# Kernel tuning notes

Measured on AMD Instinct MI355X. Metric: run time of the kernel, lower is better.

Reference implementation:

```python
import jax, jax.numpy as jnp
import numpy as np

B, N, C, K = 8, 18432, 1024, 1024  # scenes, points(=V*576 tokens), feat dim, num_sample_tokens
VOXEL_SIZE = 0.2


def setup_inputs() -> dict:
    rng = np.random.default_rng(0)
    # room-scale point cloud, ~0.2m voxels -> substantial pooling
    xyz = rng.uniform(-3.0, 3.0, size=(B, N, 3)).astype(np.float32)
    vox = np.floor(xyz / VOXEL_SIZE).astype(np.int64)
    p2v = np.zeros((B, N), dtype=np.int32)
    counts = []
    for b in range(B):  # host-side preprocessing (mirrors torch voxelize hash+unique)
        h = vox[b, :, 0] * 1_000_000 + vox[b, :, 1] * 1_000 + vox[b, :, 2]
        _, inv = np.unique(h, return_inverse=True)
        p2v[b] = inv.astype(np.int32)
        counts.append(int(inv.max()) + 1)
    S = max(counts)  # static segment count (>= per-batch voxel counts)
    # per-batch random resample over that batch's occupied voxels (np.random.choice in source)
    resample = np.stack([
        rng.choice(counts[b], size=K, replace=counts[b] < K) for b in range(B)
    ]).astype(np.int32)
    feats = jax.random.normal(jax.random.key(0), (B, N, C), dtype=jnp.float32)
    return {
        "video_features": feats,
        "p2v": jnp.asarray(p2v),
        "resample_idx": jnp.asarray(resample),
        "num_segments": S,
    }


def reference(video_features, p2v, resample_idx, num_segments):
    # scatter_mean per batch: sum features per voxel / point count per voxel
    def pool_one(f, seg):  # f: [N, C], seg: [N]
        sums = jax.ops.segment_sum(f, seg, num_segments=num_segments)          # [S, C]
        cnt = jax.ops.segment_sum(jnp.ones((f.shape[0],), f.dtype), seg,
                                  num_segments=num_segments)                    # [S]
        return sums / jnp.maximum(cnt, 1.0)[:, None]

    means = jax.vmap(pool_one)(video_features, p2v)                             # [B, S, C]
    # fixed-size resample gather -> [B, K, C]
    out = jnp.take_along_axis(means, resample_idx[..., None].astype(jnp.int32), axis=1)
    return out
```

## Files before the change

### kernel.cpp

```cpp
#include <hip/hip_runtime.h>

#define BATCH 8
#define NPTS  18432
#define CH    1024
#define KOUT  1024
#define MAXS  18432
#define CAP   64

__global__ void scatter_map_kernel(const int* __restrict__ resample,
                                   int* __restrict__ map) {
    int i = blockIdx.x * blockDim.x + threadIdx.x;
    if (i >= BATCH * KOUT) return;
    int b = i / KOUT;
    int vox = resample[i];
    map[b * MAXS + vox] = i - b * KOUT;
}

__global__ void build_lists_kernel(const int* __restrict__ p2v,
                                   const int* __restrict__ map,
                                   int* __restrict__ counts,
                                   int* __restrict__ lists) {
    int i = blockIdx.x * blockDim.x + threadIdx.x;
    if (i >= BATCH * NPTS) return;
    int b = i / NPTS;
    int vox = p2v[i];
    int slot = map[b * MAXS + vox];
    if (slot < 0) return;
    int row = b * KOUT + slot;
    int pos = atomicAdd(&counts[row], 1);
    if (pos < CAP) lists[row * CAP + pos] = i;
}

__global__ void gather_mean_kernel(const float* __restrict__ feats,
                                   const int* __restrict__ counts,
                                   const int* __restrict__ lists,
                                   float* __restrict__ out) {
    int row = blockIdx.x;
    int cnt = counts[row];
    int n = cnt < CAP ? cnt : CAP;
    float4 acc = make_float4(0.f, 0.f, 0.f, 0.f);
    for (int j = 0; j < n; ++j) {
        int pt = lists[row * CAP + j];
        float4 v = ((const float4*)(feats + (size_t)pt * CH))[threadIdx.x];
        acc.x += v.x; acc.y += v.y; acc.z += v.z; acc.w += v.w;
    }
    float inv = 1.0f / (float)(cnt > 0 ? cnt : 1);
    acc.x *= inv; acc.y *= inv; acc.z *= inv; acc.w *= inv;
    ((float4*)(out + (size_t)row * CH))[threadIdx.x] = acc;
}

extern "C" void kernel_launch(void* const* d_in, const int* in_sizes, int n_in,
                              void* d_out, int out_size, void* d_ws, size_t ws_size,
                              hipStream_t stream) {
    const float* feats    = (const float*)d_in[0];
    const int*   p2v      = (const int*)  d_in[1];
    const int*   resample = (const int*)  d_in[2];
    float* out = (float*)d_out;

    int* map    = (int*)d_ws;
    int* counts = map + BATCH * MAXS;
    int* lists  = counts + BATCH * KOUT;

    hipMemsetAsync(map,    0xFF, (size_t)BATCH * MAXS * sizeof(int), stream);
    hipMemsetAsync(counts, 0,    (size_t)BATCH * KOUT * sizeof(int), stream);

    scatter_map_kernel<<<(BATCH * KOUT + 255) / 256, 256, 0, stream>>>(resample, map);

    build_lists_kernel<<<(BATCH * NPTS + 255) / 256, 256, 0, stream>>>(
        p2v, map, counts, lists);

    gather_mean_kernel<<<BATCH * KOUT, 256, 0, stream>>>(feats, counts, lists, out);
}
```

Before: 669.3 us.

## Fuse map, list build and gather into one cooperative persistent kernel

Replaces two memsets and three kernel launches with a single cooperative kernel. It initializes the workspace, builds the voxel map, builds the point lists and performs the gather-mean, separated by grid-wide syncs. The gather now assigns one wave per output row with four float4 accumulators per lane. This removes launch and memset overheads and raises memory-level parallelism, at the cost of grid-sync latency and a fixed persistent grid size.

Result: slower. 929.1 us (+38.8%).

```diff
diff --git a/kernel.cpp b/kernel.cpp
--- a/kernel.cpp
+++ b/kernel.cpp
@@ -1,4 +1,7 @@
 #include <hip/hip_runtime.h>
+#include <hip/hip_cooperative_groups.h>
+
+namespace cg = cooperative_groups;
 
 #define BATCH 8
 #define NPTS  18432
@@ -7,46 +10,75 @@
 #define MAXS  18432
 #define CAP   64
 
-__global__ void scatter_map_kernel(const int* __restrict__ resample,
-                                   int* __restrict__ map) {
-    int i = blockIdx.x * blockDim.x + threadIdx.x;
-    if (i >= BATCH * KOUT) return;
-    int b = i / KOUT;
-    int vox = resample[i];
-    map[b * MAXS + vox] = i - b * KOUT;
-}
+#define GRID_BLOCKS   1024
+#define BLOCK_THREADS 256
 
-__global__ void build_lists_kernel(const int* __restrict__ p2v,
-                                   const int* __restrict__ map,
-                                   int* __restrict__ counts,
-                                   int* __restrict__ lists) {
-    int i = blockIdx.x * blockDim.x + threadIdx.x;
-    if (i >= BATCH * NPTS) return;
-    int b = i / NPTS;
-    int vox = p2v[i];
-    int slot = map[b * MAXS + vox];
-    if (slot < 0) return;
-    int row = b * KOUT + slot;
-    int pos = atomicAdd(&counts[row], 1);
-    if (pos < CAP) lists[row * CAP + pos] = i;
-}
+__global__ __launch_bounds__(BLOCK_THREADS, 4)
+void fused_pool_kernel(const float* __restrict__ feats,
+                       const int*   __restrict__ p2v,
+                       const int*   __restrict__ resample,
+                       int*         __restrict__ map,
+                       int*         __restrict__ counts,
+                       int*         __restrict__ lists,
+                       float*       __restrict__ out) {
+    cg::grid_group grid = cg::this_grid();
+    const int tid      = blockIdx.x * BLOCK_THREADS + threadIdx.x;
+    const int nthreads = GRID_BLOCKS * BLOCK_THREADS;
 
-__global__ void gather_mean_kernel(const float* __restrict__ feats,
-                                   const int* __restrict__ counts,
-                                   const int* __restrict__ lists,
-                                   float* __restrict__ out) {
-    int row = blockIdx.x;
-    int cnt = counts[row];
-    int n = cnt < CAP ? cnt : CAP;
-    float4 acc = make_float4(0.f, 0.f, 0.f, 0.f);
-    for (int j = 0; j < n; ++j) {
-        int pt = lists[row * CAP + j];
-        float4 v = ((const float4*)(feats + (size_t)pt * CH))[threadIdx.x];
-        acc.x += v.x; acc.y += v.y; acc.z += v.z; acc.w += v.w;
+    for (int i = tid; i < BATCH * MAXS; i += nthreads) map[i] = -1;
+    for (int i = tid; i < BATCH * KOUT; i += nthreads) counts[i] = 0;
+    grid.sync();
+
+    for (int i = tid; i < BATCH * KOUT; i += nthreads) {
+        int b = i >> 10;
+        map[b * MAXS + resample[i]] = i & (KOUT - 1);
     }
-    float inv = 1.0f / (float)(cnt > 0 ? cnt : 1);
-    acc.x *= inv; acc.y *= inv; acc.z *= inv; acc.w *= inv;
-    ((float4*)(out + (size_t)row * CH))[threadIdx.x] = acc;
+    grid.sync();
+
+    for (int i = tid; i < BATCH * NPTS; i += nthreads) {
+        int b    = i / NPTS;
+        int slot = map[b * MAXS + p2v[i]];
+        if (slot >= 0) {
+            int row = (b << 10) + slot;
+            int pos = atomicAdd(&counts[row], 1);
+            if (pos < CAP) lists[row * CAP + pos] = i;
+        }
+    }
+    grid.sync();
+
+    const int wid    = tid >> 6;
+    const int lane   = tid & 63;
+    const int nwaves = nthreads >> 6;
+    for (int row = wid; row < BATCH * KOUT; row += nwaves) {
+        int cnt = counts[row];
+        int n   = cnt < CAP ? cnt : CAP;
+        float4 a0 = make_float4(0.f, 0.f, 0.f, 0.f);
+        float4 a1 = make_float4(0.f, 0.f, 0.f, 0.f);
+        float4 a2 = make_float4(0.f, 0.f, 0.f, 0.f);
+        float4 a3 = make_float4(0.f, 0.f, 0.f, 0.f);
+        for (int j = 0; j < n; ++j) {
+            int pt = lists[row * CAP + j];
+            const float4* src = (const float4*)(feats + (size_t)pt * CH);
+            float4 v0 = src[lane];
+            float4 v1 = src[lane + 64];
+            float4 v2 = src[lane + 128];
+            float4 v3 = src[lane + 192];
+            a0.x += v0.x; a0.y += v0.y; a0.z += v0.z; a0.w += v0.w;
+            a1.x += v1.x; a1.y += v1.y; a1.z += v1.z; a1.w += v1.w;
+            a2.x += v2.x; a2.y += v2.y; a2.z += v2.z; a2.w += v2.w;
+            a3.x += v3.x; a3.y += v3.y; a3.z += v3.z; a3.w += v3.w;
+        }
+        float inv = 1.0f / (float)(cnt > 0 ? cnt : 1);
+        a0.x *= inv; a0.y *= inv; a0.z *= inv; a0.w *= inv;
+        a1.x *= inv; a1.y *= inv; a1.z *= inv; a1.w *= inv;
+        a2.x *= inv; a2.y *= inv; a2.z *= inv; a2.w *= inv;
+        a3.x *= inv; a3.y *= inv; a3.z *= inv; a3.w *= inv;
+        float4* dst = (float4*)(out + (size_t)row * CH);
+        dst[lane]       = a0;
+        dst[lane + 64]  = a1;
+        dst[lane + 128] = a2;
+        dst[lane + 192] = a3;
+    }
 }
 
 extern "C" void kernel_launch(void* const* d_in, const int* in_sizes, int n_in,
@@ -61,13 +93,11 @@
     int* counts = map + BATCH * MAXS;
     int* lists  = counts + BATCH * KOUT;
 
-    hipMemsetAsync(map,    0xFF, (size_t)BATCH * MAXS * sizeof(int), stream);
-    hipMemsetAsync(counts, 0,    (size_t)BATCH * KOUT * sizeof(int), stream);
-
-    scatter_map_kernel<<<(BATCH * KOUT + 255) / 256, 256, 0, stream>>>(resample, map);
-
-    build_lists_kernel<<<(BATCH * NPTS + 255) / 256, 256, 0, stream>>>(
-        p2v, map, counts, lists);
-
-    gather_mean_kernel<<<BATCH * KOUT, 256, 0, stream>>>(feats, counts, lists, out);
+    void* args[] = {
+        (void*)&feats, (void*)&p2v, (void*)&resample,
+        (void*)&map, (void*)&counts, (void*)&lists, (void*)&out
+    };
+    hipLaunchCooperativeKernel((const void*)fused_pool_kernel,
+                               dim3(GRID_BLOCKS), dim3(BLOCK_THREADS),
+                               args, 0, stream);
 }
```
